# Kernel optimization log

Measured on AMD Instinct MI355X. Metric: run time of the kernel, lower is better.

The kernel has to match this reference:

```python
import jax, jax.numpy as jnp
import numpy as np

D_MODEL = 1024
NHEAD = 16
D_HEAD = D_MODEL // NHEAD
B, L = 2, 2048


def setup_inputs() -> dict:
    key = jax.random.key(0)
    ks = jax.random.split(key, 11)
    s = 1.0 / np.sqrt(D_MODEL)
    return {
        "Q": jax.random.normal(ks[0], (B, L, D_MODEL), jnp.float32),
        "K": jax.random.normal(ks[1], (B, L, D_MODEL), jnp.float32),
        "V": jax.random.normal(ks[2], (B, L, D_MODEL), jnp.float32),
        "Wq": jax.random.normal(ks[3], (D_MODEL, D_MODEL), jnp.float32) * s,
        "bq": jax.random.normal(ks[4], (D_MODEL,), jnp.float32) * 0.01,
        "Wk": jax.random.normal(ks[5], (D_MODEL, D_MODEL), jnp.float32) * s,
        "bk": jax.random.normal(ks[6], (D_MODEL,), jnp.float32) * 0.01,
        "Wv": jax.random.normal(ks[7], (D_MODEL, D_MODEL), jnp.float32) * s,
        "bv": jax.random.normal(ks[8], (D_MODEL,), jnp.float32) * 0.01,
        "Wo": jax.random.normal(ks[9], (D_MODEL, D_MODEL), jnp.float32) * s,
        "bo": jax.random.normal(ks[10], (D_MODEL,), jnp.float32) * 0.01,
    }


def reference(Q, K, V, Wq, bq, Wk, bk, Wv, bv, Wo, bo):
    b, l, _ = Q.shape
    # QKV linear projections (nn.Linear: x @ W.T + b), then split into heads
    q = (Q @ Wq.T + bq).reshape(b, l, NHEAD, D_HEAD)
    k = (K @ Wk.T + bk).reshape(b, l, NHEAD, D_HEAD)
    v = (V @ Wv.T + bv).reshape(b, l, NHEAD, D_HEAD)
    # scaled dot-product attention: softmax(QK^T / sqrt(d_head)) V
    scale = jnp.asarray(1.0 / np.sqrt(D_HEAD), q.dtype)
    scores = jnp.einsum("bqhd,bkhd->bhqk", q, k) * scale  # [B,H,L,L]
    attn = jax.nn.softmax(scores, axis=-1)
    out = jnp.einsum("bhqk,bkhd->bqhd", attn, v)  # [B,L,H,Dh]
    out = out.reshape(b, l, D_MODEL)  # concat heads
    return out @ Wo.T + bo
```

## Files before the change

### kernel.cpp

```cpp
#include <hip/hip_runtime.h>
#include <cstdint>
#include <cstddef>

#define DM 1024
#define NH 16
#define DH 64
#define NB 2
#define SQ 2048
#define MT (NB*SQ)

typedef float  f32x4  __attribute__((ext_vector_type(4)));
typedef float  f32x16 __attribute__((ext_vector_type(16)));
typedef short  s16x8 __attribute__((ext_vector_type(8)));
typedef short  s16x4 __attribute__((ext_vector_type(4)));

__device__ __forceinline__ unsigned short f2bf(float x) {
    unsigned int u = __float_as_uint(x);
    unsigned int lsb = (u >> 16) & 1u;
    u += 0x7fffu + lsb;
    return (unsigned short)(u >> 16);
}

__device__ __forceinline__ unsigned int cvtpk(float lo, float hi) {
    unsigned int r;
    asm("v_cvt_pk_bf16_f32 %0, %1, %2" : "=v"(r) : "v"(lo), "v"(hi));
    return r;
}

__device__ __forceinline__ void gload16(const void* g, void* l) {
    __builtin_amdgcn_global_load_lds(
        (const __attribute__((address_space(1))) void*)g,
        (__attribute__((address_space(3))) void*)l,
        16, 0, 0);
}

__global__ __launch_bounds__(256) void castk(const float* __restrict__ in,
                                             unsigned short* __restrict__ out, int n) {
    int i = (blockIdx.x * 256 + threadIdx.x) * 4;
    if (i >= n) return;
    float4 a = *reinterpret_cast<const float4*>(in + i);
    s16x4 r;
    r[0] = (short)f2bf(a.x);
    r[1] = (short)f2bf(a.y);
    r[2] = (short)f2bf(a.z);
    r[3] = (short)f2bf(a.w);
    *reinterpret_cast<s16x4*>(out + i) = r;
}

__device__ __forceinline__ void gemm_core(const unsigned short* __restrict__ A,
                                          const unsigned short* __restrict__ Bm,
                                          int m0, int n0, int t,
                                          unsigned short (*As)[64],
                                          unsigned short (*Bs)[64],
                                          f32x4 acc[4][4]) {
    const int lane = t & 63, w = t >> 6;
    const int wm = (w >> 1) * 64, wn = (w & 1) * 64;
    const int lo = lane & 15, hi = lane >> 4;

    for (int k0 = 0; k0 < DM; k0 += 64) {
#pragma unroll
        for (int i = 0; i < 4; i++) {
            int c = i * 256 + t;
            int r = c >> 3, col = (c & 7) * 8;
            gload16(A  + (size_t)(m0 + r) * DM + k0 + col, &As[r][col]);
            gload16(Bm + (size_t)(n0 + r) * DM + k0 + col, &Bs[r][col]);
        }
        asm volatile("s_waitcnt vmcnt(0)" ::: "memory");
        __syncthreads();

#pragma unroll
        for (int kk = 0; kk < 64; kk += 32) {
            s16x8 a[4], b[4];
#pragma unroll
            for (int mi = 0; mi < 4; mi++)
                a[mi] = *reinterpret_cast<const s16x8*>(&As[wm + mi * 16 + lo][kk + hi * 8]);
#pragma unroll
            for (int ni = 0; ni < 4; ni++)
                b[ni] = *reinterpret_cast<const s16x8*>(&Bs[wn + ni * 16 + lo][kk + hi * 8]);
#pragma unroll
            for (int mi = 0; mi < 4; mi++)
#pragma unroll
                for (int ni = 0; ni < 4; ni++)
                    acc[mi][ni] = __builtin_amdgcn_mfma_f32_16x16x32_bf16(
                        a[mi], b[ni], acc[mi][ni], 0, 0, 0);
        }
        __syncthreads();
    }
}

__global__ __launch_bounds__(256, 3) void gemm_qkv(
    const unsigned short* __restrict__ Qb, const unsigned short* __restrict__ Kb,
    const unsigned short* __restrict__ Vb,
    const unsigned short* __restrict__ Wq, const unsigned short* __restrict__ Wk,
    const unsigned short* __restrict__ Wv,
    const float* __restrict__ bq, const float* __restrict__ bk, const float* __restrict__ bv,
    unsigned short* __restrict__ qp, unsigned short* __restrict__ kp,
    unsigned short* __restrict__ vt) {
    __shared__ __align__(16) unsigned short As[128][64];
    __shared__ __align__(16) unsigned short Bs[128][64];
    const int t = threadIdx.x;
    const int z = blockIdx.z;
    const unsigned short* A    = (z == 0) ? Qb : (z == 1) ? Kb : Vb;
    const unsigned short* Bm   = (z == 0) ? Wq : (z == 1) ? Wk : Wv;
    const float*          bias = (z == 0) ? bq : (z == 1) ? bk : bv;
    const int m0 = blockIdx.y * 128, n0 = blockIdx.x * 128;

    f32x4 acc[4][4] = {};
    gemm_core(A, Bm, m0, n0, t, As, Bs, acc);

    const int lane = t & 63, w = t >> 6;
    const int wm = (w >> 1) * 64, wn = (w & 1) * 64;
    const int lo = lane & 15, hi = lane >> 4;

    if (z < 2) {
        unsigned short* C = z ? kp : qp;
        const float scale = z ? 1.0f : 0.18033688011112042f;
#pragma unroll
        for (int mi = 0; mi < 4; mi++)
#pragma unroll
            for (int ni = 0; ni < 4; ni++) {
                int cc = n0 + wn + ni * 16 + lo;
                float bb = bias[cc];
#pragma unroll
                for (int j = 0; j < 4; j++) {
                    int rr = m0 + wm + mi * 16 + hi * 4 + j;
                    C[(size_t)rr * DM + cc] = f2bf((acc[mi][ni][j] + bb) * scale);
                }
            }
    } else {
#pragma unroll
        for (int mi = 0; mi < 4; mi++)
#pragma unroll
            for (int ni = 0; ni < 4; ni++) {
                int cc = n0 + wn + ni * 16 + lo;
                float bb = bias[cc];
                int rr0 = m0 + wm + mi * 16 + hi * 4;
                size_t base = ((size_t)(rr0 >> 11) * DM + cc) * SQ + (rr0 & (SQ - 1));
                s16x4 st;
#pragma unroll
                for (int j = 0; j < 4; j++)
                    st[j] = (short)f2bf(acc[mi][ni][j] + bb);
                *reinterpret_cast<s16x4*>(&vt[base]) = st;
            }
    }
}

__global__ __launch_bounds__(256, 3) void gemm_out(
    const unsigned short* __restrict__ Ao, const unsigned short* __restrict__ Wo,
    const float* __restrict__ bo, float* __restrict__ Cout) {
    __shared__ __align__(16) unsigned short As[128][64];
    __shared__ __align__(16) unsigned short Bs[128][64];
    const int t = threadIdx.x;
    const int m0 = blockIdx.y * 128, n0 = blockIdx.x * 128;

    f32x4 acc[4][4] = {};
    gemm_core(Ao, Wo, m0, n0, t, As, Bs, acc);

    const int lane = t & 63, w = t >> 6;
    const int wm = (w >> 1) * 64, wn = (w & 1) * 64;
    const int lo = lane & 15, hi = lane >> 4;
#pragma unroll
    for (int mi = 0; mi < 4; mi++)
#pragma unroll
        for (int ni = 0; ni < 4; ni++) {
            int cc = n0 + wn + ni * 16 + lo;
            float bb = bo[cc];
#pragma unroll
            for (int j = 0; j < 4; j++) {
                int rr = m0 + wm + mi * 16 + hi * 4 + j;
                Cout[(size_t)rr * DM + cc] = acc[mi][ni][j] + bb;
            }
        }
}

__global__ __launch_bounds__(256, 2) void attn_k(
    const unsigned short* __restrict__ qp, const unsigned short* __restrict__ kp,
    const unsigned short* __restrict__ vt, unsigned short* __restrict__ ao) {
    __shared__ __align__(16) unsigned short Ks[128][64];
    __shared__ __align__(16) unsigned short Vs[64][128];

    const int t = threadIdx.x;
    const int lane = t & 63, w = t >> 6;
    const int l5 = lane & 31, hb = lane >> 5;
    const int q0 = blockIdx.x * 128;
    const int bh = blockIdx.y;
    const int b = bh >> 4, h = bh & 15;

    const unsigned short* qrow = qp + (size_t)(b * SQ + q0 + w * 32 + l5) * DM + h * DH;
    s16x8 qfrag[4];
#pragma unroll
    for (int kk = 0; kk < 4; kk++)
        qfrag[kk] = *reinterpret_cast<const s16x8*>(qrow + kk * 16 + hb * 8);

    float mrow = -1e30f, lrow = 0.0f;
    f32x16 oaccT[2] = {};

    for (int kt = 0; kt < SQ; kt += 128) {
#pragma unroll
        for (int i = 0; i < 4; i++) {
            int c = i * 256 + t;
            int r = c >> 3, col = ((c & 7) ^ (r & 7)) * 8;
            gload16(kp + (size_t)(b * SQ + kt + r) * DM + h * DH + col, &Ks[r][(c & 7) * 8]);
        }
#pragma unroll
        for (int i = 0; i < 4; i++) {
            int c = i * 256 + t;
            int r = c >> 4, col = ((c & 15) ^ (r & 15)) * 8;
            gload16(vt + (size_t)(bh * DH + r) * SQ + kt + col, &Vs[r][(c & 15) * 8]);
        }
        asm volatile("s_waitcnt vmcnt(0)" ::: "memory");
        __syncthreads();

        f32x16 sT[4] = {};
        __builtin_amdgcn_s_setprio(1);
#pragma unroll
        for (int ks = 0; ks < 4; ks++) {
#pragma unroll
            for (int kk = 0; kk < 4; kk++) {
                int kr = ks * 32 + l5;
                s16x8 kf = *reinterpret_cast<const s16x8*>(
                    &Ks[kr][((kk * 2 + hb) ^ (kr & 7)) * 8]);
                sT[ks] = __builtin_amdgcn_mfma_f32_32x32x16_bf16(
                    kf, qfrag[kk], sT[ks], 0, 0, 0);
            }
        }
        __builtin_amdgcn_s_setprio(0);

        float mx = -3.0e38f;
#pragma unroll
        for (int ks = 0; ks < 4; ks++) {
            float t0 = fmaxf(fmaxf(sT[ks][0], sT[ks][1]), sT[ks][2]);
            float t1 = fmaxf(fmaxf(sT[ks][3], sT[ks][4]), sT[ks][5]);
            float t2 = fmaxf(fmaxf(sT[ks][6], sT[ks][7]), sT[ks][8]);
            float t3 = fmaxf(fmaxf(sT[ks][9], sT[ks][10]), sT[ks][11]);
            float t4 = fmaxf(fmaxf(sT[ks][12], sT[ks][13]), sT[ks][14]);
            float t5 = fmaxf(fmaxf(sT[ks][15], t0), t1);
            float t6 = fmaxf(fmaxf(t2, t3), t4);
            mx = fmaxf(fmaxf(mx, t5), t6);
        }
        mx = fmaxf(mx, __shfl_xor(mx, 32));

        if (!__all(mx <= mrow + 8.0f)) {
            float mnew = fmaxf(mrow, mx);
            float fs = exp2f(mrow - mnew);
            mrow = mnew;
            lrow *= fs;
            oaccT[0] *= fs;
            oaccT[1] *= fs;
        }

        float ps0 = 0.0f, ps1 = 0.0f, ps2 = 0.0f, ps3 = 0.0f;
#pragma unroll
        for (int ks = 0; ks < 4; ks++)
#pragma unroll
            for (int r = 0; r < 16; r += 4) {
                float e0 = exp2f(sT[ks][r]     - mrow);
                float e1 = exp2f(sT[ks][r + 1] - mrow);
                float e2 = exp2f(sT[ks][r + 2] - mrow);
                float e3 = exp2f(sT[ks][r + 3] - mrow);
                sT[ks][r] = e0; sT[ks][r + 1] = e1;
                sT[ks][r + 2] = e2; sT[ks][r + 3] = e3;
                ps0 += e0; ps1 += e1; ps2 += e2; ps3 += e3;
            }
        float ps = (ps0 + ps1) + (ps2 + ps3);
        ps += __shfl_xor(ps, 32);
        lrow += ps;

#pragma unroll
        for (int ks = 0; ks < 4; ks++) {
            unsigned int pw0[4], pw1[4];
#pragma unroll
            for (int m = 0; m < 4; m++) {
                pw0[m] = cvtpk(sT[ks][4 * m], sT[ks][4 * m + 1]);
                pw1[m] = cvtpk(sT[ks][4 * m + 2], sT[ks][4 * m + 3]);
            }
#pragma unroll
            for (int tt = 0; tt < 2; tt++) {
                unsigned int s0 = hb ? pw0[2 * tt] : pw0[2 * tt + 1];
                unsigned int s1 = hb ? pw1[2 * tt] : pw1[2 * tt + 1];
                unsigned int r0 = __shfl_xor(s0, 32);
                unsigned int r1 = __shfl_xor(s1, 32);
                union { unsigned int u[4]; s16x8 v; } uu;
                if (hb == 0) { uu.u[0] = pw0[2 * tt]; uu.u[1] = pw1[2 * tt];
                               uu.u[2] = r0;          uu.u[3] = r1; }
                else         { uu.u[0] = r0;          uu.u[1] = r1;
                               uu.u[2] = pw0[2 * tt + 1]; uu.u[3] = pw1[2 * tt + 1]; }
                s16x8 pf = uu.v;
                __builtin_amdgcn_s_setprio(1);
#pragma unroll
                for (int dblk = 0; dblk < 2; dblk++) {
                    int vr = dblk * 32 + l5;
                    int sl = ((ks * 2 + tt) * 2 + hb) ^ (vr & 15);
                    s16x8 vf = *reinterpret_cast<const s16x8*>(&Vs[vr][sl * 8]);
                    oaccT[dblk] = __builtin_amdgcn_mfma_f32_32x32x16_bf16(
                        vf, pf, oaccT[dblk], 0, 0, 0);
                }
                __builtin_amdgcn_s_setprio(0);
            }
        }
        __syncthreads();
    }

    float inv = 1.0f / lrow;
    size_t rowbase = (size_t)(b * SQ + q0 + w * 32 + l5) * DM + h * DH;
#pragma unroll
    for (int dblk = 0; dblk < 2; dblk++)
#pragma unroll
        for (int g = 0; g < 4; g++) {
            unsigned int w0 = cvtpk(oaccT[dblk][4 * g] * inv, oaccT[dblk][4 * g + 1] * inv);
            unsigned int w1 = cvtpk(oaccT[dblk][4 * g + 2] * inv, oaccT[dblk][4 * g + 3] * inv);
            uint2 st = make_uint2(w0, w1);
            *reinterpret_cast<uint2*>(&ao[rowbase + dblk * 32 + 8 * g + 4 * hb]) = st;
        }
}

extern "C" void kernel_launch(void* const* d_in, const int* in_sizes, int n_in,
                              void* d_out, int out_size, void* d_ws, size_t ws_size,
                              hipStream_t stream) {
    const float* Q  = (const float*)d_in[0];
    const float* K  = (const float*)d_in[1];
    const float* V  = (const float*)d_in[2];
    const float* Wq = (const float*)d_in[3];
    const float* bq = (const float*)d_in[4];
    const float* Wk = (const float*)d_in[5];
    const float* bk = (const float*)d_in[6];
    const float* Wv = (const float*)d_in[7];
    const float* bv = (const float*)d_in[8];
    const float* Wo = (const float*)d_in[9];
    const float* bo = (const float*)d_in[10];

    char* ws = (char*)d_ws;
    size_t off = 0;
    auto alloc = [&](size_t bytes) {
        void* p = ws + off;
        off += (bytes + 255) & ~(size_t)255;
        return p;
    };
    const size_t XB = (size_t)MT * DM * 2;
    const size_t WB = (size_t)DM * DM * 2;
    unsigned short* qb  = (unsigned short*)alloc(XB);
    unsigned short* kb  = (unsigned short*)alloc(XB);
    unsigned short* vb  = (unsigned short*)alloc(XB);
    unsigned short* wqb = (unsigned short*)alloc(WB);
    unsigned short* wkb = (unsigned short*)alloc(WB);
    unsigned short* wvb = (unsigned short*)alloc(WB);
    unsigned short* wob = (unsigned short*)alloc(WB);
    unsigned short* qp  = (unsigned short*)alloc(XB);
    unsigned short* kp  = (unsigned short*)alloc(XB);
    unsigned short* vtp = (unsigned short*)alloc(XB);
    unsigned short* ao  = (unsigned short*)alloc(XB);

    castk<<<dim3(MT * DM / 1024), 256, 0, stream>>>(Q, qb, MT * DM);
    castk<<<dim3(MT * DM / 1024), 256, 0, stream>>>(K, kb, MT * DM);
    castk<<<dim3(MT * DM / 1024), 256, 0, stream>>>(V, vb, MT * DM);
    castk<<<dim3(DM * DM / 1024), 256, 0, stream>>>(Wq, wqb, DM * DM);
    castk<<<dim3(DM * DM / 1024), 256, 0, stream>>>(Wk, wkb, DM * DM);
    castk<<<dim3(DM * DM / 1024), 256, 0, stream>>>(Wv, wvb, DM * DM);
    castk<<<dim3(DM * DM / 1024), 256, 0, stream>>>(Wo, wob, DM * DM);

    gemm_qkv<<<dim3(DM / 128, MT / 128, 3), 256, 0, stream>>>(
        qb, kb, vb, wqb, wkb, wvb, bq, bk, bv, qp, kp, vtp);

    attn_k<<<dim3(SQ / 128, NB * NH), 256, 0, stream>>>(qp, kp, vtp, ao);

    gemm_out<<<dim3(DM / 128, MT / 128), 256, 0, stream>>>(ao, wob, bo, (float*)d_out);
}
```

Before: 263.0 us.

## Double-buffer K/V tiles in attention and merge cast kernels into one launch

The attention kernel now keeps two LDS buffers for K and V and prefetches the next tile with async global-to-LDS loads while computing the current one. It waits with a partial vmcnt so only the current tile's loads must be complete. Separately, the seven fp32-to-bf16 cast launches are merged into a single kernel that picks source and destination by block index. The aims are to hide global load latency inside attention and to cut launch overhead. The cost is double the LDS in attention (64KB per block), which may limit occupancy at two blocks per CU.

```diff
diff --git a/kernel.cpp b/kernel.cpp
--- a/kernel.cpp
+++ b/kernel.cpp
@@ -34,17 +34,40 @@
         16, 0, 0);
 }
 
-__global__ __launch_bounds__(256) void castk(const float* __restrict__ in,
-                                             unsigned short* __restrict__ out, int n) {
-    int i = (blockIdx.x * 256 + threadIdx.x) * 4;
-    if (i >= n) return;
-    float4 a = *reinterpret_cast<const float4*>(in + i);
-    s16x4 r;
-    r[0] = (short)f2bf(a.x);
-    r[1] = (short)f2bf(a.y);
-    r[2] = (short)f2bf(a.z);
-    r[3] = (short)f2bf(a.w);
-    *reinterpret_cast<s16x4*>(out + i) = r;
+#define BIGB (MT*DM/1024)
+#define WB_B (DM*DM/1024)
+__global__ __launch_bounds__(256) void castall(
+    const float* __restrict__ s0, const float* __restrict__ s1, const float* __restrict__ s2,
+    const float* __restrict__ s3, const float* __restrict__ s4, const float* __restrict__ s5,
+    const float* __restrict__ s6,
+    unsigned short* __restrict__ d0, unsigned short* __restrict__ d1,
+    unsigned short* __restrict__ d2, unsigned short* __restrict__ d3,
+    unsigned short* __restrict__ d4, unsigned short* __restrict__ d5,
+    unsigned short* __restrict__ d6) {
+    int bid = blockIdx.x;
+    const float* src;
+    unsigned short* dst;
+    int off;
+    if (bid < 3 * BIGB) {
+        int seg = bid / BIGB;
+        off = (bid - seg * BIGB) * 1024;
+        src = (seg == 0) ? s0 : (seg == 1) ? s1 : s2;
+        dst = (seg == 0) ? d0 : (seg == 1) ? d1 : d2;
+    } else {
+        int r = bid - 3 * BIGB;
+        int seg = r / WB_B;
+        off = (r - seg * WB_B) * 1024;
+        src = (seg == 0) ? s3 : (seg == 1) ? s4 : (seg == 2) ? s5 : s6;
+        dst = (seg == 0) ? d3 : (seg == 1) ? d4 : (seg == 2) ? d5 : d6;
+    }
+    int i = off + threadIdx.x * 4;
+    float4 a = *reinterpret_cast<const float4*>(src + i);
+    s16x4 rr;
+    rr[0] = (short)f2bf(a.x);
+    rr[1] = (short)f2bf(a.y);
+    rr[2] = (short)f2bf(a.z);
+    rr[3] = (short)f2bf(a.w);
+    *reinterpret_cast<s16x4*>(dst + i) = rr;
 }
 
 __device__ __forceinline__ void gemm_core(const unsigned short* __restrict__ A,
@@ -176,8 +199,8 @@
 __global__ __launch_bounds__(256, 2) void attn_k(
     const unsigned short* __restrict__ qp, const unsigned short* __restrict__ kp,
     const unsigned short* __restrict__ vt, unsigned short* __restrict__ ao) {
-    __shared__ __align__(16) unsigned short Ks[128][64];
-    __shared__ __align__(16) unsigned short Vs[64][128];
+    __shared__ __align__(16) unsigned short Ks[2][128][64];
+    __shared__ __align__(16) unsigned short Vs[2][64][128];
 
     const int t = threadIdx.x;
     const int lane = t & 63, w = t >> 6;
@@ -192,24 +215,39 @@
     for (int kk = 0; kk < 4; kk++)
         qfrag[kk] = *reinterpret_cast<const s16x8*>(qrow + kk * 16 + hb * 8);
 
-    float mrow = -1e30f, lrow = 0.0f;
-    f32x16 oaccT[2] = {};
-
-    for (int kt = 0; kt < SQ; kt += 128) {
+    auto stage = [&](int bufi, int kt) {
 #pragma unroll
         for (int i = 0; i < 4; i++) {
             int c = i * 256 + t;
             int r = c >> 3, col = ((c & 7) ^ (r & 7)) * 8;
-            gload16(kp + (size_t)(b * SQ + kt + r) * DM + h * DH + col, &Ks[r][(c & 7) * 8]);
+            gload16(kp + (size_t)(b * SQ + kt + r) * DM + h * DH + col,
+                    &Ks[bufi][r][(c & 7) * 8]);
         }
 #pragma unroll
         for (int i = 0; i < 4; i++) {
             int c = i * 256 + t;
             int r = c >> 4, col = ((c & 15) ^ (r & 15)) * 8;
-            gload16(vt + (size_t)(bh * DH + r) * SQ + kt + col, &Vs[r][(c & 15) * 8]);
-        }
-        asm volatile("s_waitcnt vmcnt(0)" ::: "memory");
-        __syncthreads();
+            gload16(vt + (size_t)(bh * DH + r) * SQ + kt + col,
+                    &Vs[bufi][r][(c & 15) * 8]);
+        }
+    };
+
+    float mrow = -1e30f, lrow = 0.0f;
+    f32x16 oaccT[2] = {};
+
+    stage(0, 0);
+    int cur = 0;
+    const int NT = SQ / 128;
+
+    for (int ti = 0; ti < NT; ti++) {
+        if (ti + 1 < NT) {
+            stage(cur ^ 1, (ti + 1) * 128);
+            asm volatile("s_waitcnt vmcnt(8)" ::: "memory");
+        } else {
+            asm volatile("s_waitcnt vmcnt(0)" ::: "memory");
+        }
+        __builtin_amdgcn_sched_barrier(0);
+        __builtin_amdgcn_s_barrier();
 
         f32x16 sT[4] = {};
         __builtin_amdgcn_s_setprio(1);
@@ -219,7 +257,7 @@
             for (int kk = 0; kk < 4; kk++) {
                 int kr = ks * 32 + l5;
                 s16x8 kf = *reinterpret_cast<const s16x8*>(
-                    &Ks[kr][((kk * 2 + hb) ^ (kr & 7)) * 8]);
+                    &Ks[cur][kr][((kk * 2 + hb) ^ (kr & 7)) * 8]);
                 sT[ks] = __builtin_amdgcn_mfma_f32_32x32x16_bf16(
                     kf, qfrag[kk], sT[ks], 0, 0, 0);
             }
@@ -291,14 +329,16 @@
                 for (int dblk = 0; dblk < 2; dblk++) {
                     int vr = dblk * 32 + l5;
                     int sl = ((ks * 2 + tt) * 2 + hb) ^ (vr & 15);
-                    s16x8 vf = *reinterpret_cast<const s16x8*>(&Vs[vr][sl * 8]);
+                    s16x8 vf = *reinterpret_cast<const s16x8*>(&Vs[cur][vr][sl * 8]);
                     oaccT[dblk] = __builtin_amdgcn_mfma_f32_32x32x16_bf16(
                         vf, pf, oaccT[dblk], 0, 0, 0);
                 }
                 __builtin_amdgcn_s_setprio(0);
             }
         }
-        __syncthreads();
+
+        __builtin_amdgcn_s_barrier();
+        cur ^= 1;
     }
 
     float inv = 1.0f / lrow;
@@ -350,13 +390,8 @@
     unsigned short* vtp = (unsigned short*)alloc(XB);
     unsigned short* ao  = (unsigned short*)alloc(XB);
 
-    castk<<<dim3(MT * DM / 1024), 256, 0, stream>>>(Q, qb, MT * DM);
-    castk<<<dim3(MT * DM / 1024), 256, 0, stream>>>(K, kb, MT * DM);
-    castk<<<dim3(MT * DM / 1024), 256, 0, stream>>>(V, vb, MT * DM);
-    castk<<<dim3(DM * DM / 1024), 256, 0, stream>>>(Wq, wqb, DM * DM);
-    castk<<<dim3(DM * DM / 1024), 256, 0, stream>>>(Wk, wkb, DM * DM);
-    castk<<<dim3(DM * DM / 1024), 256, 0, stream>>>(Wv, wvb, DM * DM);
-    castk<<<dim3(DM * DM / 1024), 256, 0, stream>>>(Wo, wob, DM * DM);
+    castall<<<dim3(3 * BIGB + 4 * WB_B), 256, 0, stream>>>(
+        Q, K, V, Wq, Wk, Wv, Wo, qb, kb, vb, wqb, wkb, wvb, wob);
 
     gemm_qkv<<<dim3(DM / 128, MT / 128, 3), 256, 0, stream>>>(
         qb, kb, vb, wqb, wkb, wvb, bq, bk, bv, qp, kp, vtp);
```

Result: faster. 254.2 us (-3.3%).
